# Performance work log

Hardware: AMD Instinct MI355X
Metric: run time of the kernel (lower is better)

## Reference

```python
import jax, jax.numpy as jnp
import numpy as np

B, T, D, H, P = 2, 2048, 1024, 16, 64  # batch, seq, d_model, heads, head_dim


def setup_inputs() -> dict:
    key = jax.random.key(0)
    ks = jax.random.split(key, 8)
    s = 0.02
    return {
        "Q": jax.random.normal(ks[0], (B, T, D), jnp.float32),
        "K": jax.random.normal(ks[1], (B, T, D), jnp.float32),
        "V": jax.random.normal(ks[2], (B, T, D), jnp.float32),
        "mask": jnp.ones((B, 1, 1, T), jnp.float32),
        "WQ": jax.random.normal(ks[3], (H, D, P), jnp.float32) * s,
        "WK": jax.random.normal(ks[4], (H, D, P), jnp.float32) * s,
        "WV": jax.random.normal(ks[5], (H, D, P), jnp.float32) * s,
        "rel_emb": jax.random.normal(ks[6], (2 * T - 1, P), jnp.float32) * s,
        "dense_W": jax.random.normal(ks[7], (H * P, D), jnp.float32) * s,
        "dense_b": jnp.zeros((D,), jnp.float32),
    }


def reference(Q, K, V, mask, WQ, WK, WV, rel_emb, dense_W, dense_b):
    # multi-head projections: (B,T,D) x (H,D,P) -> (B,H,T,P)
    q = jnp.einsum("btd,hdp->bhtp", Q, WQ)
    k = jnp.einsum("btd,hdp->bhtp", K, WK)
    v = jnp.einsum("btd,hdp->bhtp", V, WV)

    Tq = q.shape[2]
    # Shaw-style additive relative positional encoding from Q:
    # bias[b,h,i,j] = q[b,h,i] . rel_emb[j - i + T - 1]
    a = jnp.einsum("bhtp,rp->bhtr", q, rel_emb)          # (B,H,T,2T-1)
    rel_idx = jnp.arange(Tq)[None, :] - jnp.arange(Tq)[:, None] + (Tq - 1)  # (T,T)
    rpe = jnp.take_along_axis(a, rel_idx[None, None], axis=-1)              # (B,H,T,T)

    scale = 1.0 / jnp.sqrt(jnp.asarray(P, q.dtype))
    energies = (jnp.einsum("bhtp,bhsp->bhts", q, k) + rpe) * scale
    energies = energies + (1.0 - mask) * -1e9
    alphas = jax.nn.softmax(energies, axis=-1)
    ctx = jnp.einsum("bhts,bhsp->bhtp", alphas, v)        # (B,H,T,P)

    ctx = jnp.transpose(ctx, (0, 2, 1, 3)).reshape(ctx.shape[0], Tq, H * P)
    return ctx @ dense_W + dense_b
```

## Files before the change

### kernel.cpp

```cpp
#include <hip/hip_runtime.h>
#include <hip/hip_bf16.h>

typedef __bf16 bf16_t;
typedef __bf16 bf16x2 __attribute__((ext_vector_type(2)));
typedef __bf16 bf16x8 __attribute__((ext_vector_type(8)));
typedef float f32x4 __attribute__((ext_vector_type(4)));

#define QSCALE 0.1803368801111396f
#define MLOG2E 1.4426950408889634f
#define MCONST 12.0f

__device__ __forceinline__ f32x4 mfma16(bf16x8 a, bf16x8 b, f32x4 c) {
  return __builtin_amdgcn_mfma_f32_16x16x32_bf16(a, b, c, 0, 0, 0);
}

#define GLDS16(gsrc, ldst)                                                     \
  __builtin_amdgcn_global_load_lds(                                            \
      (const __attribute__((address_space(1))) void*)(gsrc),                   \
      (__attribute__((address_space(3))) void*)(ldst), 16, 0, 0)

__device__ __forceinline__ unsigned pack2(float a, float b) {
  bf16x2 t = {(bf16_t)a, (bf16_t)b};
  return __builtin_bit_cast(unsigned, t);
}

__global__ void conv_kernel(const float* __restrict__ Q,
                            const float* __restrict__ K,
                            const float* __restrict__ V,
                            bf16_t* __restrict__ qf, bf16_t* __restrict__ kf,
                            bf16_t* __restrict__ vf) {
  const int y = blockIdx.y;
  const float* s = y == 0 ? Q : (y == 1 ? K : V);
  bf16_t* d = y == 0 ? qf : (y == 1 ? kf : vf);
  size_t i = ((size_t)blockIdx.x * 256 + threadIdx.x) * 8;
  float4 a = *(const float4*)(s + i);
  float4 b = *(const float4*)(s + i + 4);
  uint4 u = {pack2(a.x, a.y), pack2(a.z, a.w), pack2(b.x, b.y),
             pack2(b.z, b.w)};
  *(uint4*)(d + i) = u;
}

__global__ void transpose_w_kernel(const float* __restrict__ WQ,
                                   const float* __restrict__ WK,
                                   const float* __restrict__ WV,
                                   const float* __restrict__ dW,
                                   bf16_t* __restrict__ wqt,
                                   bf16_t* __restrict__ wkt,
                                   bf16_t* __restrict__ wvt,
                                   bf16_t* __restrict__ dwt) {
  __shared__ float tl[64][65];
  const int mat = blockIdx.y;
  const float* s = mat == 0 ? WQ : (mat == 1 ? WK : (mat == 2 ? WV : dW));
  bf16_t* d = mat == 0 ? wqt : (mat == 1 ? wkt : (mat == 2 ? wvt : dwt));
  const int tile = blockIdx.x;
  int row0, col0;
  size_t sstride;
  const float* sp;
  if (mat < 3) {
    int h = tile >> 4;
    row0 = (tile & 15) * 64;
    col0 = h * 64;
    sstride = 64;
    sp = s + (size_t)h * 65536 + (size_t)row0 * 64;
  } else {
    int nt = tile >> 4;
    row0 = (tile & 15) * 64;
    col0 = nt * 64;
    sstride = 1024;
    sp = s + (size_t)row0 * 1024 + (size_t)nt * 64;
  }
  const int t = threadIdx.x;
#pragma unroll
  for (int i = 0; i < 16; i++) {
    int lin = t + i * 256;
    int r = lin >> 6, c = lin & 63;
    tl[r][c] = sp[(size_t)r * sstride + c];
  }
  __syncthreads();
#pragma unroll
  for (int i = 0; i < 16; i++) {
    int lin = t + i * 256;
    int p = lin >> 6, k = lin & 63;
    d[(size_t)(col0 + p) * 1024 + row0 + k] = (bf16_t)tl[k][p];
  }
}

__global__ void prep_kernel(const float* __restrict__ rel,
                            const float* __restrict__ mask,
                            bf16_t* __restrict__ relb,
                            float* __restrict__ mbias) {
  int idx = blockIdx.x * 256 + threadIdx.x;
  if (idx < 4096 * 64) {
    int row = idx >> 6;
    int col = idx & 63;
    int sr = row > 4094 ? 4094 : row;
    relb[idx] = (bf16_t)rel[sr * 64 + col];
  } else {
    int j = idx - 4096 * 64;
    if (j < 4096) mbias[j] = (1.0f - mask[j]) * -1e9f * MLOG2E;
  }
}

__global__ __launch_bounds__(256) void proj_gemm_kernel(
    const bf16_t* __restrict__ Qf, const bf16_t* __restrict__ Kf,
    const bf16_t* __restrict__ Vf, const bf16_t* __restrict__ WQt,
    const bf16_t* __restrict__ WKt, const bf16_t* __restrict__ WVt,
    bf16_t* __restrict__ qb, bf16_t* __restrict__ kb,
    bf16_t* __restrict__ vb) {
  const int z = blockIdx.z;
  const bf16_t* A = z == 0 ? Qf : (z == 1 ? Kf : Vf);
  const bf16_t* Wt = z == 0 ? WQt : (z == 1 ? WKt : WVt);
  bf16_t* out = z == 0 ? qb : (z == 1 ? kb : vb);
  const float scale = z == 0 ? QSCALE : 1.0f;

  __shared__ bf16_t As[128 * 64];
  __shared__ bf16_t Bs[128 * 64];
  const int tid = threadIdx.x;
  const int lane = tid & 63;
  const int wid = tid >> 6;
  const int wm = wid >> 1, wn = wid & 1;
  const int row0 = blockIdx.x * 128;
  const int col0 = blockIdx.y * 128;
  const int lr = lane & 15;
  const int lk = (lane >> 4) * 8;
  const int srow = lane >> 3;
  const int t16 = lane & 7;
  const int swz = (lr & 7) << 3;

  f32x4 acc[4][4];
#pragma unroll
  for (int m = 0; m < 4; m++)
#pragma unroll
    for (int n = 0; n < 4; n++) acc[m][n] = {0.f, 0.f, 0.f, 0.f};

  for (int kt = 0; kt < 1024; kt += 64) {
#pragma unroll
    for (int i = 0; i < 4; i++) {
      int chunk = i * 4 + wid;
      int row = chunk * 8 + srow;
      int so = (t16 ^ (row & 7)) * 8;
      GLDS16(A + (size_t)(row0 + row) * 1024 + kt + so,
             As + chunk * 512 + lane * 8);
      GLDS16(Wt + (size_t)(col0 + row) * 1024 + kt + so,
             Bs + chunk * 512 + lane * 8);
    }
    __syncthreads();
#pragma unroll
    for (int kk = 0; kk < 2; kk++) {
      int cbs = (kk * 32 + lk) ^ swz;
      bf16x8 af[4], bfr[4];
#pragma unroll
      for (int m = 0; m < 4; m++)
        af[m] = *(const bf16x8*)&As[(wm * 64 + m * 16 + lr) * 64 + cbs];
#pragma unroll
      for (int n = 0; n < 4; n++)
        bfr[n] = *(const bf16x8*)&Bs[(wn * 64 + n * 16 + lr) * 64 + cbs];
#pragma unroll
      for (int m = 0; m < 4; m++)
#pragma unroll
        for (int n = 0; n < 4; n++)
          acc[m][n] = mfma16(af[m], bfr[n], acc[m][n]);
    }
    __syncthreads();
  }
  const int rb = (lane >> 4) * 4;
#pragma unroll
  for (int m = 0; m < 4; m++) {
#pragma unroll
    for (int n = 0; n < 4; n++) {
      int col = col0 + wn * 64 + n * 16 + lr;
      int h = col >> 6, p = col & 63;
      int row_base = row0 + wm * 64 + m * 16 + rb;
      int b = row_base >> 11, t0 = row_base & 2047;
      if (z == 2) {
        uint2 u = {pack2(acc[m][n][0], acc[m][n][1]),
                   pack2(acc[m][n][2], acc[m][n][3])};
        *(uint2*)&out[(((size_t)(b * 16 + h) * 64 + p) * 2048) + t0] = u;
      } else {
#pragma unroll
        for (int r = 0; r < 4; r++) {
          out[(((size_t)(b * 16 + h) * 2048 + t0 + r) * 64) + p] =
              (bf16_t)(acc[m][n][r] * scale);
        }
      }
    }
  }
}

__global__ __launch_bounds__(256) void dense_gemm_kernel(
    const bf16_t* __restrict__ A, const bf16_t* __restrict__ Wt,
    const float* __restrict__ bias, float* __restrict__ out) {
  __shared__ bf16_t As[128 * 64];
  __shared__ bf16_t Bs[128 * 64];
  const int tid = threadIdx.x;
  const int lane = tid & 63;
  const int wid = tid >> 6;
  const int wm = wid >> 1, wn = wid & 1;
  const int row0 = blockIdx.x * 128;
  const int col0 = blockIdx.y * 128;
  const int lr = lane & 15;
  const int lk = (lane >> 4) * 8;
  const int srow = lane >> 3;
  const int t16 = lane & 7;
  const int swz = (lr & 7) << 3;

  f32x4 acc[4][4];
#pragma unroll
  for (int m = 0; m < 4; m++)
#pragma unroll
    for (int n = 0; n < 4; n++) acc[m][n] = {0.f, 0.f, 0.f, 0.f};

  for (int kt = 0; kt < 1024; kt += 64) {
#pragma unroll
    for (int i = 0; i < 4; i++) {
      int chunk = i * 4 + wid;
      int row = chunk * 8 + srow;
      int so = (t16 ^ (row & 7)) * 8;
      GLDS16(A + (size_t)(row0 + row) * 1024 + kt + so,
             As + chunk * 512 + lane * 8);
      GLDS16(Wt + (size_t)(col0 + row) * 1024 + kt + so,
             Bs + chunk * 512 + lane * 8);
    }
    __syncthreads();
#pragma unroll
    for (int kk = 0; kk < 2; kk++) {
      int cbs = (kk * 32 + lk) ^ swz;
      bf16x8 af[4], bfr[4];
#pragma unroll
      for (int m = 0; m < 4; m++)
        af[m] = *(const bf16x8*)&As[(wm * 64 + m * 16 + lr) * 64 + cbs];
#pragma unroll
      for (int n = 0; n < 4; n++)
        bfr[n] = *(const bf16x8*)&Bs[(wn * 64 + n * 16 + lr) * 64 + cbs];
#pragma unroll
      for (int m = 0; m < 4; m++)
#pragma unroll
        for (int n = 0; n < 4; n++)
          acc[m][n] = mfma16(af[m], bfr[n], acc[m][n]);
    }
    __syncthreads();
  }
  const int rb = (lane >> 4) * 4;
#pragma unroll
  for (int m = 0; m < 4; m++) {
#pragma unroll
    for (int n = 0; n < 4; n++) {
      int col = col0 + wn * 64 + n * 16 + lr;
      float bv = bias[col];
#pragma unroll
      for (int r = 0; r < 4; r++) {
        int row = row0 + wm * 64 + m * 16 + rb + r;
        out[(size_t)row * 1024 + col] = acc[m][n][r] + bv;
      }
    }
  }
}

__global__ __launch_bounds__(256, 2) void attn_kernel(
    const bf16_t* __restrict__ qg, const bf16_t* __restrict__ kg,
    const bf16_t* __restrict__ vt, const bf16_t* __restrict__ relb,
    const float* __restrict__ mbias, bf16_t* __restrict__ ctx) {
  __shared__ bf16_t Kb[2][64 * 64];
  __shared__ bf16_t Vb[2][64 * 64];
  __shared__ bf16_t Rr[4][64 * 64];
  __shared__ unsigned SC[4][688];

  const int tid = threadIdx.x;
  const int lane = tid & 63;
  const int w = tid >> 6;

  const int id = blockIdx.x;
  const int id2 = (id & 7) * 64 + (id >> 3);
  const int it = id2 & 15;
  const int bh = id2 >> 4;
  const int h = bh & 15;
  const int b = bh >> 4;
  const int i0 = it * 128;

  const size_t base = ((size_t)bh) * 2048 * 64;
  const int lr = lane & 15;
  const int g = lane >> 4;
  const int lk = g * 8;
  const int srow = lane >> 3;
  const int t16 = lane & 7;
  const int swz = (lr & 7) << 3;

  const bf16_t* kgb = kg + base;
  const bf16_t* vgb = vt + base;
  const bf16_t* rgb = relb + (size_t)(1920 - i0) * 64;

  bf16x8 aq[2][2];
#pragma unroll
  for (int gq = 0; gq < 2; gq++) {
    const bf16_t* src =
        qg + base + (size_t)(i0 + w * 32 + gq * 16 + lr) * 64 + lk;
    aq[gq][0] = *(const bf16x8*)(src);
    aq[gq][1] = *(const bf16x8*)(src + 32);
  }

  float l0 = 0.f, l1 = 0.f;
  f32x4 o0[4], o1[4];
#pragma unroll
  for (int n = 0; n < 4; n++) {
    o0[n] = {0.f, 0.f, 0.f, 0.f};
    o1[n] = {0.f, 0.f, 0.f, 0.f};
  }

  const float* mb_base = mbias + (size_t)b * 2048;
  unsigned* scw = SC[w];
  int sh[4];
#pragma unroll
  for (int r = 0; r < 4; r++) sh[r] = ((r + lr + 1) & 1) << 4;

#pragma unroll
  for (int i = 0; i < 2; i++) {
    int chunk = i * 4 + w;
    int row = chunk * 8 + srow;
    GLDS16(kgb + row * 64 + ((t16 ^ (row & 7)) * 8),
           Kb[0] + chunk * 512 + lane * 8);
  }
#pragma unroll
  for (int i = 0; i < 2; i++) {
    int chunk = i * 4 + w;
    int p = chunk * 8 + srow;
    GLDS16(vgb + (size_t)p * 2048 + ((t16 ^ (p & 7)) * 8),
           Vb[0] + chunk * 512 + lane * 8);
  }
#pragma unroll
  for (int c = 0; c < 3; c++) {
#pragma unroll
    for (int i = 0; i < 2; i++) {
      int chunk = i * 4 + w;
      int row = chunk * 8 + srow;
      GLDS16(rgb + (size_t)(c * 64 + row) * 64 + ((t16 ^ (row & 7)) * 8),
             Rr[c] + chunk * 512 + lane * 8);
    }
  }
  __syncthreads();

  for (int jt = 0; jt < 32; jt++) {
    const int j0 = jt * 64;

    f32x4 mbv[4];
#pragma unroll
    for (int n = 0; n < 4; n++)
      mbv[n] = *(const f32x4*)&mb_base[j0 + n * 16 + g * 4];

    if (jt < 31) {
#pragma unroll
      for (int i = 0; i < 2; i++) {
        int chunk = i * 4 + w;
        int p = chunk * 8 + srow;
        GLDS16(vgb + (j0 + 64) + (size_t)p * 2048 + ((t16 ^ (p & 7)) * 8),
               Vb[(jt + 1) & 1] + chunk * 512 + lane * 8);
      }
      const bf16_t* kn = kgb + (size_t)(j0 + 64) * 64;
      bf16_t* kd = Kb[(jt + 1) & 1];
#pragma unroll
      for (int i = 0; i < 2; i++) {
        int chunk = i * 4 + w;
        int row = chunk * 8 + srow;
        GLDS16(kn + row * 64 + ((t16 ^ (row & 7)) * 8),
               kd + chunk * 512 + lane * 8);
      }
      const bf16_t* rs = rgb + (size_t)(jt + 3) * 64 * 64;
      bf16_t* rd = Rr[(jt + 3) & 3];
#pragma unroll
      for (int i = 0; i < 2; i++) {
        int chunk = i * 4 + w;
        int row = chunk * 8 + srow;
        GLDS16(rs + row * 64 + ((t16 ^ (row & 7)) * 8),
               rd + chunk * 512 + lane * 8);
      }
    }

    f32x4 sacc0[4], sacc1[4], er0[5], er1[5];
#pragma unroll
    for (int n = 0; n < 4; n++) {
      sacc0[n] = {0.f, 0.f, 0.f, 0.f};
      sacc1[n] = {0.f, 0.f, 0.f, 0.f};
    }
#pragma unroll
    for (int n = 0; n < 5; n++) {
      er0[n] = {0.f, 0.f, 0.f, 0.f};
      er1[n] = {0.f, 0.f, 0.f, 0.f};
    }
    const bf16_t* kcur = Kb[jt & 1];
    __builtin_amdgcn_s_setprio(1);
#pragma unroll
    for (int kk = 0; kk < 2; kk++) {
      int cbs = (kk * 32 + lk) ^ swz;
#pragma unroll
      for (int n = 0; n < 4; n++) {
        bf16x8 ak = *(const bf16x8*)&kcur[(n * 16 + lr) * 64 + cbs];
        sacc0[n] = mfma16(ak, aq[0][kk], sacc0[n]);
        sacc1[n] = mfma16(ak, aq[1][kk], sacc1[n]);
      }
#pragma unroll
      for (int fi = 0; fi < 6; fi++) {
        int f = 6 - 2 * w + fi;
        const bf16_t* rc = Rr[(jt + (f >> 2)) & 3];
        bf16x8 ar = *(const bf16x8*)&rc[((f & 3) * 16 + lr) * 64 + cbs];
        if (fi >= 1) er0[fi - 1] = mfma16(ar, aq[0][kk], er0[fi - 1]);
        if (fi <= 4) er1[fi] = mfma16(ar, aq[1][kk], er1[fi]);
      }
    }
    __builtin_amdgcn_s_setprio(0);

    const bf16_t* vcur = Vb[jt & 1];
    bf16x8 av[2][4];

    {
#pragma unroll
      for (int n2 = 0; n2 < 5; n2++) {
        uint2 u = {pack2(er0[n2][0], er0[n2][1]), pack2(er0[n2][2], er0[n2][3])};
        *(uint2*)&scw[lr * 42 + n2 * 8 + g * 2] = u;
      }
      float ps = 0.f;
      float e[4][4];
#pragma unroll
      for (int n = 0; n < 4; n++) {
#pragma unroll
        for (int r = 0; r < 4; r++) {
          int key = n * 16 + g * 4 + r;
          int idx = key - lr + 15;
          unsigned d = scw[lr * 42 + (idx >> 1)];
          float bias = __builtin_bit_cast(float, (d >> sh[r]) << 16);
          float s = sacc0[n][r] + bias + mbv[n][r];
          e[n][r] = exp2f(s - MCONST);
          ps += e[n][r];
        }
      }
      l0 += ps;
#pragma unroll
      for (int n = 0; n < 4; n++) {
        uint2 u = {pack2(e[n][0], e[n][1]), pack2(e[n][2], e[n][3])};
        *(uint2*)&scw[lr * 36 + n * 8 + g * 2] = u;
      }
      bf16x8 bp0[2];
      bp0[0] = __builtin_bit_cast(bf16x8, *(const uint4*)&scw[lr * 36 + g * 4]);
      bp0[1] =
          __builtin_bit_cast(bf16x8, *(const uint4*)&scw[lr * 36 + 16 + g * 4]);
#pragma unroll
      for (int kk = 0; kk < 2; kk++) {
        int cbs = (kk * 32 + lk) ^ swz;
#pragma unroll
        for (int n = 0; n < 4; n++)
          av[kk][n] = *(const bf16x8*)&vcur[(n * 16 + lr) * 64 + cbs];
      }
      __builtin_amdgcn_s_setprio(1);
#pragma unroll
      for (int kk = 0; kk < 2; kk++)
#pragma unroll
        for (int n = 0; n < 4; n++) o0[n] = mfma16(av[kk][n], bp0[kk], o0[n]);
      __builtin_amdgcn_s_setprio(0);
    }

    {
#pragma unroll
      for (int n2 = 0; n2 < 5; n2++) {
        uint2 u = {pack2(er1[n2][0], er1[n2][1]), pack2(er1[n2][2], er1[n2][3])};
        *(uint2*)&scw[lr * 42 + n2 * 8 + g * 2] = u;
      }
      float ps = 0.f;
      float e[4][4];
#pragma unroll
      for (int n = 0; n < 4; n++) {
#pragma unroll
        for (int r = 0; r < 4; r++) {
          int key = n * 16 + g * 4 + r;
          int idx = key - lr + 15;
          unsigned d = scw[lr * 42 + (idx >> 1)];
          float bias = __builtin_bit_cast(float, (d >> sh[r]) << 16);
          float s = sacc1[n][r] + bias + mbv[n][r];
          e[n][r] = exp2f(s - MCONST);
          ps += e[n][r];
        }
      }
      l1 += ps;
#pragma unroll
      for (int n = 0; n < 4; n++) {
        uint2 u = {pack2(e[n][0], e[n][1]), pack2(e[n][2], e[n][3])};
        *(uint2*)&scw[lr * 36 + n * 8 + g * 2] = u;
      }
      bf16x8 bp1[2];
      bp1[0] = __builtin_bit_cast(bf16x8, *(const uint4*)&scw[lr * 36 + g * 4]);
      bp1[1] =
          __builtin_bit_cast(bf16x8, *(const uint4*)&scw[lr * 36 + 16 + g * 4]);
      __builtin_amdgcn_s_setprio(1);
#pragma unroll
      for (int kk = 0; kk < 2; kk++)
#pragma unroll
        for (int n = 0; n < 4; n++) o1[n] = mfma16(av[kk][n], bp1[kk], o1[n]);
      __builtin_amdgcn_s_setprio(0);
    }

    __syncthreads();
  }

  l0 += __shfl_xor(l0, 16, 64);
  l0 += __shfl_xor(l0, 32, 64);
  l1 += __shfl_xor(l1, 16, 64);
  l1 += __shfl_xor(l1, 32, 64);

#pragma unroll
  for (int gq = 0; gq < 2; gq++) {
    f32x4* o = gq ? o1 : o0;
    float inv = 1.0f / (gq ? l1 : l0);
    size_t bt = (size_t)b * 2048 + i0 + w * 32 + gq * 16 + lr;
#pragma unroll
    for (int n = 0; n < 4; n++) {
      uint2 u = {pack2(o[n][0] * inv, o[n][1] * inv),
                 pack2(o[n][2] * inv, o[n][3] * inv)};
      *(uint2*)&ctx[bt * 1024 + h * 64 + n * 16 + g * 4] = u;
    }
  }
}

extern "C" void kernel_launch(void* const* d_in, const int* in_sizes, int n_in,
                              void* d_out, int out_size, void* d_ws,
                              size_t ws_size, hipStream_t stream) {
  (void)in_sizes; (void)n_in; (void)out_size; (void)ws_size;
  const float* Q    = (const float*)d_in[0];
  const float* K    = (const float*)d_in[1];
  const float* V    = (const float*)d_in[2];
  const float* mask = (const float*)d_in[3];
  const float* WQ   = (const float*)d_in[4];
  const float* WK   = (const float*)d_in[5];
  const float* WV   = (const float*)d_in[6];
  const float* rel  = (const float*)d_in[7];
  const float* dW   = (const float*)d_in[8];
  const float* db   = (const float*)d_in[9];
  float* out = (float*)d_out;

  const size_t N4M = (size_t)4096 * 1024;
  const size_t N1M = (size_t)1024 * 1024;
  bf16_t* qf   = (bf16_t*)d_ws;
  bf16_t* kf   = qf + N4M;
  bf16_t* vf   = kf + N4M;
  bf16_t* wqt  = vf + N4M;
  bf16_t* wkt  = wqt + N1M;
  bf16_t* wvt  = wkt + N1M;
  bf16_t* dwt  = wvt + N1M;
  bf16_t* qb   = dwt + N1M;
  bf16_t* kb   = qb + N4M;
  bf16_t* vb   = kb + N4M;
  bf16_t* ctxb = vb + N4M;
  bf16_t* relb = ctxb + N4M;
  float*  mbias = (float*)(relb + 4096 * 64);

  dim3 blk(256);
  conv_kernel<<<dim3(2048, 3), blk, 0, stream>>>(Q, K, V, qf, kf, vf);
  transpose_w_kernel<<<dim3(256, 4), blk, 0, stream>>>(WQ, WK, WV, dW, wqt,
                                                       wkt, wvt, dwt);
  prep_kernel<<<dim3((4096 * 64 + 4096) / 256), blk, 0, stream>>>(rel, mask,
                                                                  relb, mbias);
  proj_gemm_kernel<<<dim3(32, 8, 3), blk, 0, stream>>>(qf, kf, vf, wqt, wkt,
                                                       wvt, qb, kb, vb);
  attn_kernel<<<dim3(512), blk, 0, stream>>>(qb, kb, vb, relb, mbias, ctxb);
  dense_gemm_kernel<<<dim3(32, 8), blk, 0, stream>>>(ctxb, dwt, db, out);
}
```

Measured before the change: 186.7 us.

## Fuse fp32-to-bf16 input conversion into projection GEMM and shrink dense tiles

Drops the separate conversion kernel. The projection GEMM now loads fp32 Q/K/V directly, converts them to bf16 in registers and writes them swizzled into shared memory, which removes a full bf16 write and reread of the activations. The cost is that synchronous register loads replace the async global-to-LDS path for A, and each projection block rereads its fp32 rows across eight column tiles. Separately, the dense GEMM uses 128x64 tiles with twice as many blocks, for better occupancy of the 256-CU device.

Result: faster. 181.3 us (-2.9%).

```diff
diff --git a/kernel.cpp b/kernel.cpp
--- a/kernel.cpp
+++ b/kernel.cpp
@@ -22,22 +22,6 @@
 __device__ __forceinline__ unsigned pack2(float a, float b) {
   bf16x2 t = {(bf16_t)a, (bf16_t)b};
   return __builtin_bit_cast(unsigned, t);
-}
-
-__global__ void conv_kernel(const float* __restrict__ Q,
-                            const float* __restrict__ K,
-                            const float* __restrict__ V,
-                            bf16_t* __restrict__ qf, bf16_t* __restrict__ kf,
-                            bf16_t* __restrict__ vf) {
-  const int y = blockIdx.y;
-  const float* s = y == 0 ? Q : (y == 1 ? K : V);
-  bf16_t* d = y == 0 ? qf : (y == 1 ? kf : vf);
-  size_t i = ((size_t)blockIdx.x * 256 + threadIdx.x) * 8;
-  float4 a = *(const float4*)(s + i);
-  float4 b = *(const float4*)(s + i + 4);
-  uint4 u = {pack2(a.x, a.y), pack2(a.z, a.w), pack2(b.x, b.y),
-             pack2(b.z, b.w)};
-  *(uint4*)(d + i) = u;
 }
 
 __global__ void transpose_w_kernel(const float* __restrict__ WQ,
@@ -102,13 +86,13 @@
 }
 
 __global__ __launch_bounds__(256) void proj_gemm_kernel(
-    const bf16_t* __restrict__ Qf, const bf16_t* __restrict__ Kf,
-    const bf16_t* __restrict__ Vf, const bf16_t* __restrict__ WQt,
+    const float* __restrict__ Q, const float* __restrict__ K,
+    const float* __restrict__ V, const bf16_t* __restrict__ WQt,
     const bf16_t* __restrict__ WKt, const bf16_t* __restrict__ WVt,
     bf16_t* __restrict__ qb, bf16_t* __restrict__ kb,
     bf16_t* __restrict__ vb) {
   const int z = blockIdx.z;
-  const bf16_t* A = z == 0 ? Qf : (z == 1 ? Kf : Vf);
+  const float* A = z == 0 ? Q : (z == 1 ? K : V);
   const bf16_t* Wt = z == 0 ? WQt : (z == 1 ? WKt : WVt);
   bf16_t* out = z == 0 ? qb : (z == 1 ? kb : vb);
   const float scale = z == 0 ? QSCALE : 1.0f;
@@ -139,10 +123,20 @@
       int chunk = i * 4 + wid;
       int row = chunk * 8 + srow;
       int so = (t16 ^ (row & 7)) * 8;
-      GLDS16(A + (size_t)(row0 + row) * 1024 + kt + so,
-             As + chunk * 512 + lane * 8);
       GLDS16(Wt + (size_t)(col0 + row) * 1024 + kt + so,
              Bs + chunk * 512 + lane * 8);
+    }
+#pragma unroll
+    for (int i = 0; i < 4; i++) {
+      int c = tid + i * 256;
+      int row = c >> 3;
+      int k8 = (c & 7) * 8;
+      const float* src = A + (size_t)(row0 + row) * 1024 + kt + k8;
+      float4 v0 = *(const float4*)(src);
+      float4 v1 = *(const float4*)(src + 4);
+      uint4 u = {pack2(v0.x, v0.y), pack2(v0.z, v0.w), pack2(v1.x, v1.y),
+                 pack2(v1.z, v1.w)};
+      *(uint4*)&As[row * 64 + (k8 ^ ((row & 7) << 3))] = u;
     }
     __syncthreads();
 #pragma unroll
@@ -191,22 +185,21 @@
     const bf16_t* __restrict__ A, const bf16_t* __restrict__ Wt,
     const float* __restrict__ bias, float* __restrict__ out) {
   __shared__ bf16_t As[128 * 64];
-  __shared__ bf16_t Bs[128 * 64];
+  __shared__ bf16_t Bs[64 * 64];
   const int tid = threadIdx.x;
   const int lane = tid & 63;
   const int wid = tid >> 6;
-  const int wm = wid >> 1, wn = wid & 1;
   const int row0 = blockIdx.x * 128;
-  const int col0 = blockIdx.y * 128;
+  const int col0 = blockIdx.y * 64;
   const int lr = lane & 15;
   const int lk = (lane >> 4) * 8;
   const int srow = lane >> 3;
   const int t16 = lane & 7;
   const int swz = (lr & 7) << 3;
 
-  f32x4 acc[4][4];
-#pragma unroll
-  for (int m = 0; m < 4; m++)
+  f32x4 acc[2][4];
+#pragma unroll
+  for (int m = 0; m < 2; m++)
 #pragma unroll
     for (int n = 0; n < 4; n++) acc[m][n] = {0.f, 0.f, 0.f, 0.f};
 
@@ -218,6 +211,12 @@
       int so = (t16 ^ (row & 7)) * 8;
       GLDS16(A + (size_t)(row0 + row) * 1024 + kt + so,
              As + chunk * 512 + lane * 8);
+    }
+#pragma unroll
+    for (int i = 0; i < 2; i++) {
+      int chunk = i * 4 + wid;
+      int row = chunk * 8 + srow;
+      int so = (t16 ^ (row & 7)) * 8;
       GLDS16(Wt + (size_t)(col0 + row) * 1024 + kt + so,
              Bs + chunk * 512 + lane * 8);
     }
@@ -225,15 +224,15 @@
 #pragma unroll
     for (int kk = 0; kk < 2; kk++) {
       int cbs = (kk * 32 + lk) ^ swz;
-      bf16x8 af[4], bfr[4];
-#pragma unroll
-      for (int m = 0; m < 4; m++)
-        af[m] = *(const bf16x8*)&As[(wm * 64 + m * 16 + lr) * 64 + cbs];
+      bf16x8 af[2], bfr[4];
+#pragma unroll
+      for (int m = 0; m < 2; m++)
+        af[m] = *(const bf16x8*)&As[(wid * 32 + m * 16 + lr) * 64 + cbs];
 #pragma unroll
       for (int n = 0; n < 4; n++)
-        bfr[n] = *(const bf16x8*)&Bs[(wn * 64 + n * 16 + lr) * 64 + cbs];
-#pragma unroll
-      for (int m = 0; m < 4; m++)
+        bfr[n] = *(const bf16x8*)&Bs[(n * 16 + lr) * 64 + cbs];
+#pragma unroll
+      for (int m = 0; m < 2; m++)
 #pragma unroll
         for (int n = 0; n < 4; n++)
           acc[m][n] = mfma16(af[m], bfr[n], acc[m][n]);
@@ -242,14 +241,14 @@
   }
   const int rb = (lane >> 4) * 4;
 #pragma unroll
-  for (int m = 0; m < 4; m++) {
+  for (int m = 0; m < 2; m++) {
 #pragma unroll
     for (int n = 0; n < 4; n++) {
-      int col = col0 + wn * 64 + n * 16 + lr;
+      int col = col0 + n * 16 + lr;
       float bv = bias[col];
 #pragma unroll
       for (int r = 0; r < 4; r++) {
-        int row = row0 + wm * 64 + m * 16 + rb + r;
+        int row = row0 + wid * 32 + m * 16 + rb + r;
         out[(size_t)row * 1024 + col] = acc[m][n][r] + bv;
       }
     }
@@ -535,10 +534,7 @@
 
   const size_t N4M = (size_t)4096 * 1024;
   const size_t N1M = (size_t)1024 * 1024;
-  bf16_t* qf   = (bf16_t*)d_ws;
-  bf16_t* kf   = qf + N4M;
-  bf16_t* vf   = kf + N4M;
-  bf16_t* wqt  = vf + N4M;
+  bf16_t* wqt  = (bf16_t*)d_ws;
   bf16_t* wkt  = wqt + N1M;
   bf16_t* wvt  = wkt + N1M;
   bf16_t* dwt  = wvt + N1M;
@@ -550,13 +546,12 @@
   float*  mbias = (float*)(relb + 4096 * 64);
 
   dim3 blk(256);
-  conv_kernel<<<dim3(2048, 3), blk, 0, stream>>>(Q, K, V, qf, kf, vf);
   transpose_w_kernel<<<dim3(256, 4), blk, 0, stream>>>(WQ, WK, WV, dW, wqt,
                                                        wkt, wvt, dwt);
   prep_kernel<<<dim3((4096 * 64 + 4096) / 256), blk, 0, stream>>>(rel, mask,
                                                                   relb, mbias);
-  proj_gemm_kernel<<<dim3(32, 8, 3), blk, 0, stream>>>(qf, kf, vf, wqt, wkt,
-                                                       wvt, qb, kb, vb);
+  proj_gemm_kernel<<<dim3(32, 8, 3), blk, 0, stream>>>(Q, K, V, wqt, wkt, wvt,
+                                                       qb, kb, vb);
   attn_kernel<<<dim3(512), blk, 0, stream>>>(qb, kb, vb, relb, mbias, ctxb);
-  dense_gemm_kernel<<<dim3(32, 8), blk, 0, stream>>>(ctxb, dwt, db, out);
-}
+  dense_gemm_kernel<<<dim3(32, 16), blk, 0, stream>>>(ctxb, dwt, db, out);
+}
```
